# Performance work log

Measured on AMD Instinct MI355X. Metric: run time of the kernel, lower is better.

## Reference

```python
import jax, jax.numpy as jnp
import numpy as np

D_MODEL = 1024
N_HEADS = 16
D_HEAD = D_MODEL // N_HEADS
LATENT = 32
NEG = -1e9


def setup_inputs() -> dict:
    key = jax.random.key(0)
    ks = jax.random.split(key, 6)
    B, T = 2, 4096
    x = jax.random.normal(ks[0], (B, T, D_MODEL), dtype=jnp.float32)
    s = lambda fan_in: 1.0 / np.sqrt(fan_in)
    W_kv = jax.random.normal(ks[1], (D_MODEL, LATENT), dtype=jnp.float32) * s(D_MODEL)
    W_k = jax.random.normal(ks[2], (LATENT, D_MODEL), dtype=jnp.float32) * s(LATENT)
    W_v = jax.random.normal(ks[3], (LATENT, D_MODEL), dtype=jnp.float32) * s(LATENT)
    W_q = jax.random.normal(ks[4], (D_MODEL, D_MODEL), dtype=jnp.float32) * s(D_MODEL)
    W_o = jax.random.normal(ks[5], (D_MODEL, D_MODEL), dtype=jnp.float32) * s(D_MODEL)
    return {"x": x, "W_kv": W_kv, "W_k": W_k, "W_v": W_v, "W_q": W_q, "W_o": W_o}


def reference(x, W_kv, W_k, W_v, W_q, W_o):
    B, T, _ = x.shape
    # low-rank latent compression of KV path
    lat = jnp.einsum('btd,dl->btl', x, W_kv)              # [B,T,latent]
    def sp(t):  # [B,T,D] -> [B,H,T,dh]
        return t.reshape(B, T, N_HEADS, D_HEAD).transpose(0, 2, 1, 3)
    K = sp(jnp.einsum('btl,ld->btd', lat, W_k))
    V = sp(jnp.einsum('btl,ld->btd', lat, W_v))
    Q = sp(jnp.einsum('btd,de->bte', x, W_q))
    scale = 1.0 / jnp.sqrt(jnp.float32(D_HEAD))
    s = jnp.einsum('bhqd,bhkd->bhqk', Q, K) * scale       # [B,H,T,T]
    causal = jnp.tril(jnp.ones((T, T), dtype=jnp.float32))
    s = s + (1.0 - causal) * NEG
    attn = jax.nn.softmax(s, axis=-1)
    out = jnp.einsum('bhqk,bhkd->bhqd', attn, V)          # [B,H,T,dh]
    out = out.transpose(0, 2, 1, 3).reshape(B, T, D_MODEL)
    return jnp.einsum('btd,de->bte', out, W_o)
```

## Files before the change

### kernel.cpp

```cpp
#include <hip/hip_runtime.h>
#include <hip/hip_bf16.h>


#define T_SEQ  4096
#define NHEAD  16
#define DHEAD  64
#define DMODEL 1024
#define LATENT 32
#define BATCH  2
#define M_ROWS (BATCH * T_SEQ)

typedef __attribute__((ext_vector_type(8))) short bf16x8;
typedef __attribute__((ext_vector_type(4))) float f32x4;

__device__ __forceinline__ short f2bf(float f) {
  __hip_bfloat16 h = __float2bfloat16(f);
  return __builtin_bit_cast(short, h);
}

__device__ __forceinline__ float exp2_hw(float x) {
  return __builtin_amdgcn_exp2f(x);
}

__device__ __forceinline__ void gld_lds16(const short* g, short* l) {
  __builtin_amdgcn_global_load_lds(
      (const __attribute__((address_space(1))) void*)g,
      (__attribute__((address_space(3))) void*)l, 16, 0, 0);
}

__global__ __launch_bounds__(256)
void prep_weights(const float* __restrict__ Wq, const float* __restrict__ Wk,
                  const float* __restrict__ Wv, const float* __restrict__ Wo,
                  const float* __restrict__ Wkv, const float* __restrict__ x,
                  short* __restrict__ WcombT, short* __restrict__ WvoT,
                  short* __restrict__ xbf) {
  const int blk = blockIdx.x;
  const int tid = threadIdx.x;

  if (blk >= 256) {
    const int i = ((blk - 256) * 256 + tid) * 4;
    if (i < M_ROWS * DMODEL) {
      const f32x4 v = *(const f32x4*)(x + i);
      short4 o;
      o.x = f2bf(v[0]); o.y = f2bf(v[1]); o.z = f2bf(v[2]); o.w = f2bf(v[3]);
      *(short4*)(xbf + i) = o;
    }
    return;
  }

  if (blk < 64) {
    __shared__ float wk[32 * 64];
    const int h   = blk >> 2;
    const int dm0 = (blk & 3) * 256;
    {
      const int l  = tid >> 3;
      const int d0 = (tid & 7) * 8;
      *(f32x4*)(wk + l * 64 + d0)     = *(const f32x4*)(Wk + (size_t)l * DMODEL + h * 64 + d0);
      *(f32x4*)(wk + l * 64 + d0 + 4) = *(const f32x4*)(Wk + (size_t)l * DMODEL + h * 64 + d0 + 4);
    }
    __syncthreads();
    const int dm = dm0 + tid;
    float acc[32] = {};
    for (int dv = 0; dv < 16; ++dv) {
      const f32x4 wq = *(const f32x4*)(Wq + (size_t)dm * DMODEL + h * 64 + dv * 4);
#pragma unroll
      for (int jj = 0; jj < 4; ++jj)
#pragma unroll
        for (int l = 0; l < 32; ++l)
          acc[l] += wq[jj] * wk[l * 64 + dv * 4 + jj];
    }
    const float SCALE = 0.1803368801111f;
#pragma unroll
    for (int l = 0; l < 32; ++l)
      WcombT[((size_t)(h * 32 + l)) * DMODEL + dm] = f2bf(acc[l] * SCALE);
  } else if (blk < 128) {
    __shared__ float wvs[32 * 64];
    const int h  = (blk - 64) >> 2;
    const int n0 = ((blk - 64) & 3) * 256;
    {
      const int l  = tid >> 3;
      const int d0 = (tid & 7) * 8;
      *(f32x4*)(wvs + l * 64 + d0)     = *(const f32x4*)(Wv + (size_t)l * DMODEL + h * 64 + d0);
      *(f32x4*)(wvs + l * 64 + d0 + 4) = *(const f32x4*)(Wv + (size_t)l * DMODEL + h * 64 + d0 + 4);
    }
    __syncthreads();
    const int n = n0 + tid;
    float acc[32] = {};
    for (int d = 0; d < 64; ++d) {
      const float wo = Wo[(size_t)(h * 64 + d) * DMODEL + n];
#pragma unroll
      for (int l = 0; l < 32; ++l)
        acc[l] += wvs[l * 64 + d] * wo;
    }
#pragma unroll
    for (int l = 0; l < 32; ++l)
      WvoT[(size_t)n * 512 + h * 32 + l] = f2bf(acc[l]);
  } else {
    const int i = (blk - 128) * 256 + tid;
    const int k = i >> 5;
    const int l = i & 31;
    WcombT[(size_t)(512 + l) * DMODEL + k] = f2bf(Wkv[(size_t)k * LATENT + l]);
    short* z = WcombT + (size_t)544 * DMODEL + (size_t)i * 3;
    z[0] = 0; z[1] = 0; z[2] = 0;
  }
}

__global__ __launch_bounds__(256)
void gemm128_kernel(const short* __restrict__ A, const short* __restrict__ Bt,
                    short* __restrict__ Cs, float* __restrict__ Cf,
                    short* __restrict__ Cs2, short* __restrict__ Cs3,
                    int M, int K, int N, int out_mode) {
  __shared__ short Alds[128 * 32];
  __shared__ short Blds[128 * 32];

  const int tid  = threadIdx.x;
  const int wv   = tid >> 6;
  const int lane = tid & 63;
  const int quad = lane >> 4;
  const int l16  = lane & 15;
  const int wm   = wv >> 1;
  const int wn   = wv & 1;

  const int nb  = N >> 7;
  const int nwg = gridDim.x;
  int bid = blockIdx.x;
  if ((nwg & 7) == 0)
    bid = (bid & 7) * (nwg >> 3) + (bid >> 3);
  const int mt = bid / nb;
  const int nt = bid - mt * nb;
  const int m0 = mt << 7;
  const int n0 = nt << 7;

  const int rl  = lane >> 2;
  const int cl  = lane & 3;
  const int csw = cl ^ ((rl >> 1) & 3);
  const int ra  = wv * 16 + rl;
  const short* Ag0 = A  + (size_t)(m0 + ra) * K + csw * 8;
  const short* Ag1 = A  + (size_t)(m0 + 64 + ra) * K + csw * 8;
  const short* Bg0 = Bt + (size_t)(n0 + ra) * K + csw * 8;
  const short* Bg1 = Bt + (size_t)(n0 + 64 + ra) * K + csw * 8;
  short* Al0 = &Alds[(wv * 16) * 32];
  short* Al1 = &Alds[(64 + wv * 16) * 32];
  short* Bl0 = &Blds[(wv * 16) * 32];
  short* Bl1 = &Blds[(64 + wv * 16) * 32];

  const int rsw = (l16 >> 1) & 3;
  const int coff = (quad ^ rsw) * 8;

  f32x4 acc[4][4] = {};

  for (int k0 = 0; k0 < K; k0 += 32) {
    gld_lds16(Ag0 + k0, Al0);
    gld_lds16(Ag1 + k0, Al1);
    gld_lds16(Bg0 + k0, Bl0);
    gld_lds16(Bg1 + k0, Bl1);
    __builtin_amdgcn_s_waitcnt(0x0F70);
    __syncthreads();

    bf16x8 af[4], bfr[4];
#pragma unroll
    for (int i = 0; i < 4; ++i) {
      const int rowA = wm * 64 + i * 16 + l16;
      const int rowB = wn * 64 + i * 16 + l16;
      af[i]  = *(const bf16x8*)&Alds[rowA * 32 + coff];
      bfr[i] = *(const bf16x8*)&Blds[rowB * 32 + coff];
    }
#pragma unroll
    for (int i = 0; i < 4; ++i)
#pragma unroll
      for (int j = 0; j < 4; ++j)
        acc[i][j] = __builtin_amdgcn_mfma_f32_16x16x32_bf16(af[i], bfr[j], acc[i][j], 0, 0, 0);
    __syncthreads();
  }

#pragma unroll
  for (int i = 0; i < 4; ++i) {
    const int row = m0 + wm * 64 + i * 16 + quad * 4;
#pragma unroll
    for (int j = 0; j < 4; ++j) {
      const int col = n0 + wn * 64 + j * 16 + l16;
#pragma unroll
      for (int r = 0; r < 4; ++r) {
        if (out_mode == 3) {
          Cf[(size_t)(row + r) * N + col] = acc[i][j][r];
        } else {
          if (col < 512) {
            Cs[(size_t)(row + r) * 512 + col] = f2bf(acc[i][j][r]);
          } else if (col < 544) {
            const short v = f2bf(acc[i][j][r]);
            const int l = col - 512;
            const int m = row + r;
            Cs2[(size_t)m * LATENT + l] = v;
            const int bb = m >> 12;
            const int tt = m & (T_SEQ - 1);
            Cs3[((size_t)(bb * LATENT + l) << 12) + tt] = v;
          }
        }
      }
    }
  }
}

__global__ __launch_bounds__(256, 4)
void attn_kernel(const short* __restrict__ Qlat, short* __restrict__ Olat,
                 const short* __restrict__ latg, const short* __restrict__ latTg) {
  __shared__ short Klds[64 * 32];
  __shared__ short Vlds[32 * 64];
  __shared__ short Plds[4][2][16 * 72];

  const int tid  = threadIdx.x;
  const int wv   = tid >> 6;
  const int lane = tid & 63;
  const int quad = lane >> 4;
  const int l16  = lane & 15;

  const int idx = blockIdx.x;
  const int xcd = idx & 7;
  const int j   = idx >> 3;
  const int bhg = xcd * 2 + (j & 1);
  const int jj  = j >> 1;
  const int a   = jj >> 4;
  const int r_  = jj & 15;
  const int qb  = (a & 1) ? ((a == 1 ? 0 : 16) + r_) : ((a == 0 ? 63 : 47) - r_);
  const int b   = bhg >> 3;
  const int hg  = bhg & 7;

  const int q0 = qb * 64;
  const int qw = q0 + wv * 16;
  const int q  = qw + l16;

  const int srK = wv * 16 + (lane >> 2);
  const int scK = (lane & 3) ^ ((srK >> 1) & 3);
  const short* Ksrc = latg + ((size_t)b * T_SEQ + srK) * LATENT + scK * 8;
  const int srV = wv * 8 + (lane >> 3);
  const int scV = (lane & 7) ^ (srV & 7);
  const short* Vsrc = latTg + ((size_t)b * LATENT + srV) * T_SEQ + scV * 8;

  const short* Qrow = Qlat + ((size_t)(b * T_SEQ) + qw + l16) * 512 + hg * 64;
  const bf16x8 qfA = *(const bf16x8*)(Qrow + quad * 8);
  const bf16x8 qfB = *(const bf16x8*)(Qrow + 32 + quad * 8);

  bf16x8 ones;
#pragma unroll
  for (int i = 0; i < 8; ++i) ones[i] = (short)0x3F80;

  f32x4 oA[2] = {}, oB[2] = {};
  f32x4 laccA = {}, laccB = {};
  short* PA = &Plds[wv][0][0];
  short* PB = &Plds[wv][1][0];

  auto kv_step = [&](const int k0, const bool diag) {
    gld_lds16(Ksrc + (size_t)k0 * LATENT, &Klds[(wv * 16) * 32]);
    gld_lds16(Vsrc + k0,                  &Vlds[(wv * 8) * 64]);
    __builtin_amdgcn_s_waitcnt(0x0F70);
    __syncthreads();

    f32x4 sa[4], sb[4];
    __builtin_amdgcn_s_setprio(1);
#pragma unroll
    for (int mt = 0; mt < 4; ++mt) {
      if (diag && mt > wv) {
        sa[mt][0] = sa[mt][1] = sa[mt][2] = sa[mt][3] = -1e9f;
        sb[mt] = sa[mt];
        continue;
      }
      const int R = mt * 16 + l16;
      const bf16x8 kf = *(const bf16x8*)&Klds[R * 32 + ((quad ^ ((R >> 1) & 3))) * 8];
      f32x4 z = {};
      sa[mt] = __builtin_amdgcn_mfma_f32_16x16x32_bf16(kf, qfA, z, 0, 0, 0);
      sb[mt] = __builtin_amdgcn_mfma_f32_16x16x32_bf16(kf, qfB, z, 0, 0, 0);
    }
    __builtin_amdgcn_s_setprio(0);

    if (diag) {
#pragma unroll
      for (int mt = 0; mt < 4; ++mt)
#pragma unroll
        for (int r = 0; r < 4; ++r) {
          const int key = k0 + mt * 16 + quad * 4 + r;
          if (key > q) { sa[mt][r] = -1e9f; sb[mt][r] = -1e9f; }
        }
    }

#pragma unroll
    for (int mt = 0; mt < 4; ++mt)
#pragma unroll
      for (int r = 0; r < 4; ++r) {
        sa[mt][r] = exp2_hw(sa[mt][r]);
        sb[mt][r] = exp2_hw(sb[mt][r]);
      }

    asm volatile("" ::: "memory");
#pragma unroll
    for (int mt = 0; mt < 4; ++mt) {
      short4 wA, wB;
      wA.x = f2bf(sa[mt][0]); wA.y = f2bf(sa[mt][1]);
      wA.z = f2bf(sa[mt][2]); wA.w = f2bf(sa[mt][3]);
      *(short4*)(PA + l16 * 72 + mt * 16 + quad * 4) = wA;
      wB.x = f2bf(sb[mt][0]); wB.y = f2bf(sb[mt][1]);
      wB.z = f2bf(sb[mt][2]); wB.w = f2bf(sb[mt][3]);
      *(short4*)(PB + l16 * 72 + mt * 16 + quad * 4) = wB;
    }
    asm volatile("" ::: "memory");
    __builtin_amdgcn_s_waitcnt(0xC07F);
    asm volatile("" ::: "memory");
    const bf16x8 pfA0 = *(const bf16x8*)(PA + l16 * 72 + quad * 8);
    const bf16x8 pfA1 = *(const bf16x8*)(PA + l16 * 72 + 32 + quad * 8);
    const bf16x8 pfB0 = *(const bf16x8*)(PB + l16 * 72 + quad * 8);
    const bf16x8 pfB1 = *(const bf16x8*)(PB + l16 * 72 + 32 + quad * 8);
    asm volatile("" ::: "memory");

    __builtin_amdgcn_s_setprio(1);
#pragma unroll
    for (int f = 0; f < 2; ++f) {
      const int R = f * 16 + l16;
      const bf16x8 vf0 = *(const bf16x8*)&Vlds[R * 64 + ((quad    ) ^ (R & 7)) * 8];
      const bf16x8 vf1 = *(const bf16x8*)&Vlds[R * 64 + ((quad + 4) ^ (R & 7)) * 8];
      oA[f] = __builtin_amdgcn_mfma_f32_16x16x32_bf16(vf0, pfA0, oA[f], 0, 0, 0);
      oA[f] = __builtin_amdgcn_mfma_f32_16x16x32_bf16(vf1, pfA1, oA[f], 0, 0, 0);
      oB[f] = __builtin_amdgcn_mfma_f32_16x16x32_bf16(vf0, pfB0, oB[f], 0, 0, 0);
      oB[f] = __builtin_amdgcn_mfma_f32_16x16x32_bf16(vf1, pfB1, oB[f], 0, 0, 0);
    }
    laccA = __builtin_amdgcn_mfma_f32_16x16x32_bf16(ones, pfA0, laccA, 0, 0, 0);
    laccA = __builtin_amdgcn_mfma_f32_16x16x32_bf16(ones, pfA1, laccA, 0, 0, 0);
    laccB = __builtin_amdgcn_mfma_f32_16x16x32_bf16(ones, pfB0, laccB, 0, 0, 0);
    laccB = __builtin_amdgcn_mfma_f32_16x16x32_bf16(ones, pfB1, laccB, 0, 0, 0);
    __builtin_amdgcn_s_setprio(0);
    __syncthreads();
  };

#pragma unroll 1
  for (int k0 = 0; k0 < q0; k0 += 64) kv_step(k0, false);
  kv_step(q0, true);

  const float invA = 1.0f / laccA[0];
  const float invB = 1.0f / laccB[0];
  short* Orow = Olat + ((size_t)(b * T_SEQ) + qw + l16) * 512 + hg * 64;
#pragma unroll
  for (int f = 0; f < 2; ++f) {
    short4 wA, wB;
    wA.x = f2bf(oA[f][0] * invA); wA.y = f2bf(oA[f][1] * invA);
    wA.z = f2bf(oA[f][2] * invA); wA.w = f2bf(oA[f][3] * invA);
    *(short4*)(Orow + f * 16 + quad * 4) = wA;
    wB.x = f2bf(oB[f][0] * invB); wB.y = f2bf(oB[f][1] * invB);
    wB.z = f2bf(oB[f][2] * invB); wB.w = f2bf(oB[f][3] * invB);
    *(short4*)(Orow + 32 + f * 16 + quad * 4) = wB;
  }
}

extern "C" void kernel_launch(void* const* d_in, const int* in_sizes, int n_in,
                              void* d_out, int out_size, void* d_ws, size_t ws_size,
                              hipStream_t stream) {
  const float* x   = (const float*)d_in[0];
  const float* Wkv = (const float*)d_in[1];
  const float* Wk  = (const float*)d_in[2];
  const float* Wv  = (const float*)d_in[3];
  const float* Wq  = (const float*)d_in[4];
  const float* Wo  = (const float*)d_in[5];

  char* p = (char*)d_ws;
  auto carve = [&](size_t n) {
    char* r = p;
    p += (n + 255) & ~(size_t)255;
    return r;
  };
  short* xbf    = (short*)carve((size_t)M_ROWS * DMODEL * 2);
  short* Qlat   = (short*)carve((size_t)M_ROWS * 512 * 2);
  short* Olat   = (short*)carve((size_t)M_ROWS * 512 * 2);
  short* lat    = (short*)carve((size_t)M_ROWS * LATENT * 2);
  short* latT   = (short*)carve((size_t)M_ROWS * LATENT * 2);
  short* WcombT = (short*)carve((size_t)640 * DMODEL * 2);
  short* WvoT   = (short*)carve((size_t)DMODEL * 512 * 2);

  prep_weights<<<256 + M_ROWS * DMODEL / 4 / 256, 256, 0, stream>>>(
      Wq, Wk, Wv, Wo, Wkv, x, WcombT, WvoT, xbf);

  gemm128_kernel<<<(M_ROWS / 128) * (640 / 128), 256, 0, stream>>>(
      xbf, WcombT, Qlat, nullptr, lat, latT, M_ROWS, DMODEL, 640, 5);

  attn_kernel<<<1024, 256, 0, stream>>>(Qlat, Olat, lat, latT);

  gemm128_kernel<<<(M_ROWS / 128) * (DMODEL / 128), 256, 0, stream>>>(
      Olat, WvoT, nullptr, (float*)d_out, nullptr, nullptr, M_ROWS, 512, DMODEL, 3);
}
```

Before: 140.9 us.

## Process four latent-query column chunks per attention block to reuse K/V tiles

Each attention block now handles 128 columns of the latent query (four 32-wide chunks) instead of 64, so every K/V latent tile loaded into LDS feeds twice as many MFMAs, and the grid is halved to 512 blocks. The block-to-work mapping is simplified to a reversed/forward ordering of query blocks with batch and head quarter taken from the XCD index. This cuts redundant K/V global loads and barrier overhead per unit of work, but raises register and LDS use (launch bounds lowered to 2 blocks per SM) and reduces the number of blocks available for load balancing the causal triangle.

```diff
diff --git a/kernel.cpp b/kernel.cpp
--- a/kernel.cpp
+++ b/kernel.cpp
@@ -201,12 +201,12 @@
   }
 }
 
-__global__ __launch_bounds__(256, 4)
+__global__ __launch_bounds__(256, 2)
 void attn_kernel(const short* __restrict__ Qlat, short* __restrict__ Olat,
                  const short* __restrict__ latg, const short* __restrict__ latTg) {
   __shared__ short Klds[64 * 32];
   __shared__ short Vlds[32 * 64];
-  __shared__ short Plds[4][2][16 * 72];
+  __shared__ short Plds[4][4][16 * 72];
 
   const int tid  = threadIdx.x;
   const int wv   = tid >> 6;
@@ -217,13 +217,9 @@
   const int idx = blockIdx.x;
   const int xcd = idx & 7;
   const int j   = idx >> 3;
-  const int bhg = xcd * 2 + (j & 1);
-  const int jj  = j >> 1;
-  const int a   = jj >> 4;
-  const int r_  = jj & 15;
-  const int qb  = (a & 1) ? ((a == 1 ? 0 : 16) + r_) : ((a == 0 ? 63 : 47) - r_);
-  const int b   = bhg >> 3;
-  const int hg  = bhg & 7;
+  const int qb  = (j < 32) ? (63 - j) : (j - 32);
+  const int b   = xcd >> 2;
+  const int hq  = xcd & 3;
 
   const int q0 = qb * 64;
   const int qw = q0 + wv * 16;
@@ -236,18 +232,18 @@
   const int scV = (lane & 7) ^ (srV & 7);
   const short* Vsrc = latTg + ((size_t)b * LATENT + srV) * T_SEQ + scV * 8;
 
-  const short* Qrow = Qlat + ((size_t)(b * T_SEQ) + qw + l16) * 512 + hg * 64;
-  const bf16x8 qfA = *(const bf16x8*)(Qrow + quad * 8);
-  const bf16x8 qfB = *(const bf16x8*)(Qrow + 32 + quad * 8);
+  const short* Qrow = Qlat + ((size_t)(b * T_SEQ) + qw + l16) * 512 + hq * 128;
+  bf16x8 qf[4];
+#pragma unroll
+  for (int c = 0; c < 4; ++c)
+    qf[c] = *(const bf16x8*)(Qrow + c * 32 + quad * 8);
 
   bf16x8 ones;
 #pragma unroll
   for (int i = 0; i < 8; ++i) ones[i] = (short)0x3F80;
 
-  f32x4 oA[2] = {}, oB[2] = {};
-  f32x4 laccA = {}, laccB = {};
-  short* PA = &Plds[wv][0][0];
-  short* PB = &Plds[wv][1][0];
+  f32x4 o[4][2] = {};
+  f32x4 lacc[4] = {};
 
   auto kv_step = [&](const int k0, const bool diag) {
     gld_lds16(Ksrc + (size_t)k0 * LATENT, &Klds[(wv * 16) * 32]);
@@ -255,20 +251,22 @@
     __builtin_amdgcn_s_waitcnt(0x0F70);
     __syncthreads();
 
-    f32x4 sa[4], sb[4];
+    f32x4 s[4][4];
     __builtin_amdgcn_s_setprio(1);
 #pragma unroll
     for (int mt = 0; mt < 4; ++mt) {
       if (diag && mt > wv) {
-        sa[mt][0] = sa[mt][1] = sa[mt][2] = sa[mt][3] = -1e9f;
-        sb[mt] = sa[mt];
+#pragma unroll
+        for (int c = 0; c < 4; ++c)
+          s[c][mt][0] = s[c][mt][1] = s[c][mt][2] = s[c][mt][3] = -1e9f;
         continue;
       }
       const int R = mt * 16 + l16;
       const bf16x8 kf = *(const bf16x8*)&Klds[R * 32 + ((quad ^ ((R >> 1) & 3))) * 8];
       f32x4 z = {};
-      sa[mt] = __builtin_amdgcn_mfma_f32_16x16x32_bf16(kf, qfA, z, 0, 0, 0);
-      sb[mt] = __builtin_amdgcn_mfma_f32_16x16x32_bf16(kf, qfB, z, 0, 0, 0);
+#pragma unroll
+      for (int c = 0; c < 4; ++c)
+        s[c][mt] = __builtin_amdgcn_mfma_f32_16x16x32_bf16(kf, qf[c], z, 0, 0, 0);
     }
     __builtin_amdgcn_s_setprio(0);
 
@@ -278,36 +276,40 @@
 #pragma unroll
         for (int r = 0; r < 4; ++r) {
           const int key = k0 + mt * 16 + quad * 4 + r;
-          if (key > q) { sa[mt][r] = -1e9f; sb[mt][r] = -1e9f; }
+          if (key > q) {
+#pragma unroll
+            for (int c = 0; c < 4; ++c) s[c][mt][r] = -1e9f;
+          }
         }
     }
 
 #pragma unroll
-    for (int mt = 0; mt < 4; ++mt)
-#pragma unroll
-      for (int r = 0; r < 4; ++r) {
-        sa[mt][r] = exp2_hw(sa[mt][r]);
-        sb[mt][r] = exp2_hw(sb[mt][r]);
+    for (int c = 0; c < 4; ++c)
+#pragma unroll
+      for (int mt = 0; mt < 4; ++mt)
+#pragma unroll
+        for (int r = 0; r < 4; ++r)
+          s[c][mt][r] = exp2_hw(s[c][mt][r]);
+
+    asm volatile("" ::: "memory");
+#pragma unroll
+    for (int c = 0; c < 4; ++c)
+#pragma unroll
+      for (int mt = 0; mt < 4; ++mt) {
+        short4 w;
+        w.x = f2bf(s[c][mt][0]); w.y = f2bf(s[c][mt][1]);
+        w.z = f2bf(s[c][mt][2]); w.w = f2bf(s[c][mt][3]);
+        *(short4*)(&Plds[wv][c][0] + l16 * 72 + mt * 16 + quad * 4) = w;
       }
-
-    asm volatile("" ::: "memory");
-#pragma unroll
-    for (int mt = 0; mt < 4; ++mt) {
-      short4 wA, wB;
-      wA.x = f2bf(sa[mt][0]); wA.y = f2bf(sa[mt][1]);
-      wA.z = f2bf(sa[mt][2]); wA.w = f2bf(sa[mt][3]);
-      *(short4*)(PA + l16 * 72 + mt * 16 + quad * 4) = wA;
-      wB.x = f2bf(sb[mt][0]); wB.y = f2bf(sb[mt][1]);
-      wB.z = f2bf(sb[mt][2]); wB.w = f2bf(sb[mt][3]);
-      *(short4*)(PB + l16 * 72 + mt * 16 + quad * 4) = wB;
-    }
     asm volatile("" ::: "memory");
     __builtin_amdgcn_s_waitcnt(0xC07F);
     asm volatile("" ::: "memory");
-    const bf16x8 pfA0 = *(const bf16x8*)(PA + l16 * 72 + quad * 8);
-    const bf16x8 pfA1 = *(const bf16x8*)(PA + l16 * 72 + 32 + quad * 8);
-    const bf16x8 pfB0 = *(const bf16x8*)(PB + l16 * 72 + quad * 8);
-    const bf16x8 pfB1 = *(const bf16x8*)(PB + l16 * 72 + 32 + quad * 8);
+    bf16x8 pf[4][2];
+#pragma unroll
+    for (int c = 0; c < 4; ++c) {
+      pf[c][0] = *(const bf16x8*)(&Plds[wv][c][0] + l16 * 72 + quad * 8);
+      pf[c][1] = *(const bf16x8*)(&Plds[wv][c][0] + l16 * 72 + 32 + quad * 8);
+    }
     asm volatile("" ::: "memory");
 
     __builtin_amdgcn_s_setprio(1);
@@ -316,15 +318,17 @@
       const int R = f * 16 + l16;
       const bf16x8 vf0 = *(const bf16x8*)&Vlds[R * 64 + ((quad    ) ^ (R & 7)) * 8];
       const bf16x8 vf1 = *(const bf16x8*)&Vlds[R * 64 + ((quad + 4) ^ (R & 7)) * 8];
-      oA[f] = __builtin_amdgcn_mfma_f32_16x16x32_bf16(vf0, pfA0, oA[f], 0, 0, 0);
-      oA[f] = __builtin_amdgcn_mfma_f32_16x16x32_bf16(vf1, pfA1, oA[f], 0, 0, 0);
-      oB[f] = __builtin_amdgcn_mfma_f32_16x16x32_bf16(vf0, pfB0, oB[f], 0, 0, 0);
-      oB[f] = __builtin_amdgcn_mfma_f32_16x16x32_bf16(vf1, pfB1, oB[f], 0, 0, 0);
-    }
-    laccA = __builtin_amdgcn_mfma_f32_16x16x32_bf16(ones, pfA0, laccA, 0, 0, 0);
-    laccA = __builtin_amdgcn_mfma_f32_16x16x32_bf16(ones, pfA1, laccA, 0, 0, 0);
-    laccB = __builtin_amdgcn_mfma_f32_16x16x32_bf16(ones, pfB0, laccB, 0, 0, 0);
-    laccB = __builtin_amdgcn_mfma_f32_16x16x32_bf16(ones, pfB1, laccB, 0, 0, 0);
+#pragma unroll
+      for (int c = 0; c < 4; ++c) {
+        o[c][f] = __builtin_amdgcn_mfma_f32_16x16x32_bf16(vf0, pf[c][0], o[c][f], 0, 0, 0);
+        o[c][f] = __builtin_amdgcn_mfma_f32_16x16x32_bf16(vf1, pf[c][1], o[c][f], 0, 0, 0);
+      }
+    }
+#pragma unroll
+    for (int c = 0; c < 4; ++c) {
+      lacc[c] = __builtin_amdgcn_mfma_f32_16x16x32_bf16(ones, pf[c][0], lacc[c], 0, 0, 0);
+      lacc[c] = __builtin_amdgcn_mfma_f32_16x16x32_bf16(ones, pf[c][1], lacc[c], 0, 0, 0);
+    }
     __builtin_amdgcn_s_setprio(0);
     __syncthreads();
   };
@@ -333,18 +337,17 @@
   for (int k0 = 0; k0 < q0; k0 += 64) kv_step(k0, false);
   kv_step(q0, true);
 
-  const float invA = 1.0f / laccA[0];
-  const float invB = 1.0f / laccB[0];
-  short* Orow = Olat + ((size_t)(b * T_SEQ) + qw + l16) * 512 + hg * 64;
-#pragma unroll
-  for (int f = 0; f < 2; ++f) {
-    short4 wA, wB;
-    wA.x = f2bf(oA[f][0] * invA); wA.y = f2bf(oA[f][1] * invA);
-    wA.z = f2bf(oA[f][2] * invA); wA.w = f2bf(oA[f][3] * invA);
-    *(short4*)(Orow + f * 16 + quad * 4) = wA;
-    wB.x = f2bf(oB[f][0] * invB); wB.y = f2bf(oB[f][1] * invB);
-    wB.z = f2bf(oB[f][2] * invB); wB.w = f2bf(oB[f][3] * invB);
-    *(short4*)(Orow + 32 + f * 16 + quad * 4) = wB;
+  short* Orow = Olat + ((size_t)(b * T_SEQ) + qw + l16) * 512 + hq * 128;
+#pragma unroll
+  for (int c = 0; c < 4; ++c) {
+    const float inv = 1.0f / lacc[c][0];
+#pragma unroll
+    for (int f = 0; f < 2; ++f) {
+      short4 w;
+      w.x = f2bf(o[c][f][0] * inv); w.y = f2bf(o[c][f][1] * inv);
+      w.z = f2bf(o[c][f][2] * inv); w.w = f2bf(o[c][f][3] * inv);
+      *(short4*)(Orow + c * 32 + f * 16 + quad * 4) = w;
+    }
   }
 }
 
@@ -378,7 +381,7 @@
   gemm128_kernel<<<(M_ROWS / 128) * (640 / 128), 256, 0, stream>>>(
       xbf, WcombT, Qlat, nullptr, lat, latT, M_ROWS, DMODEL, 640, 5);
 
-  attn_kernel<<<1024, 256, 0, stream>>>(Qlat, Olat, lat, latT);
+  attn_kernel<<<512, 256, 0, stream>>>(Qlat, Olat, lat, latT);
 
   gemm128_kernel<<<(M_ROWS / 128) * (DMODEL / 128), 256, 0, stream>>>(
       Olat, WvoT, nullptr, (float*)d_out, nullptr, nullptr, M_ROWS, 512, DMODEL, 3);
```

New measurement: 162.9 us. 1.16x slower.
